# Kernel optimization log

Measured on AMD Instinct MI355X. Metric: run time of the kernel, lower is better.

## Reference

```python
import jax, jax.numpy as jnp
import numpy as np

H = 125      # LSTM hidden per direction
MLP = 100    # hidden_MLP
N = 1024     # sentence length


def _lstm_dir(x, wih, whh, bih, bhh, reverse):
    # x: [n, din]; torch gate order i, f, g, o
    b = bih + bhh
    def step(carry, xt):
        h, c = carry
        g = xt @ wih.T + h @ whh.T + b
        i, f, gg, o = jnp.split(g, 4)
        c = jax.nn.sigmoid(f) * c + jax.nn.sigmoid(i) * jnp.tanh(gg)
        h = jax.nn.sigmoid(o) * jnp.tanh(c)
        return (h, c), h
    z = jnp.zeros((H,), x.dtype)
    _, hs = jax.lax.scan(step, (z, z), x, reverse=reverse)
    return hs  # [n, H]


def _bilstm(x, pf, pb):
    return jnp.concatenate([_lstm_dir(x, *pf, reverse=False),
                            _lstm_dir(x, *pb, reverse=True)], axis=-1)


def setup_inputs() -> dict:
    key = jax.random.key(0)
    ks = iter(jax.random.split(key, 32))
    p = lambda shape, s=0.1: jax.random.normal(next(ks), shape, jnp.float32) * s
    inp = {}
    inp["word_idx"] = jax.random.randint(next(ks), (1, N), 0, 15948)
    inp["pos_idx"] = jax.random.randint(next(ks), (1, N), 0, 47)
    inp["true_tree_heads"] = jax.random.randint(next(ks), (N,), 0, N)
    inp["word_emb"] = p((15948, 100), 1.0)
    inp["pos_emb"] = p((47, 25), 1.0)
    for l, din in ((0, 125), (1, 250)):
        for d in ("f", "b"):
            inp[f"w_ih_{l}{d}"] = p((4 * H, din))
            inp[f"w_hh_{l}{d}"] = p((4 * H, H))
            inp[f"b_ih_{l}{d}"] = p((4 * H,))
            inp[f"b_hh_{l}{d}"] = p((4 * H,))
    inp["w1"] = p((MLP, 2 * H)); inp["b1"] = p((MLP,))
    inp["w2"] = p((MLP, 2 * H)); inp["b2"] = p((MLP,))
    inp["w3"] = p((MLP,)); inp["b3"] = p(())
    return inp


def reference(word_idx, pos_idx, true_tree_heads, word_emb, pos_emb,
              w_ih_0f, w_hh_0f, b_ih_0f, b_hh_0f,
              w_ih_0b, w_hh_0b, b_ih_0b, b_hh_0b,
              w_ih_1f, w_hh_1f, b_ih_1f, b_hh_1f,
              w_ih_1b, w_hh_1b, b_ih_1b, b_hh_1b,
              w1, b1, w2, b2, w3, b3):
    # embeddings: [n, 125]
    emb = jnp.concatenate([word_emb[word_idx[0]], pos_emb[pos_idx[0]]], axis=-1)
    h0 = _bilstm(emb, (w_ih_0f, w_hh_0f, b_ih_0f, b_hh_0f),
                 (w_ih_0b, w_hh_0b, b_ih_0b, b_hh_0b))            # [n, 250]
    h1 = _bilstm(h0, (w_ih_1f, w_hh_1f, b_ih_1f, b_hh_1f),
                 (w_ih_1b, w_hh_1b, b_ih_1b, b_hh_1b))            # [n, 250]
    heads = h1 @ w1.T + b1   # [n, 100]
    mods = h1 @ w2.T + b2    # [n, 100]
    # tag_scores[h, m] = layer3(tanh(heads[h] + mods[m])), diagonal = -inf
    s = jnp.tanh(heads[:, None, :] + mods[None, :, :])            # [n, n, 100]
    scores = jnp.einsum('hmd,d->hm', s, w3) + b3
    n = scores.shape[0]
    return jnp.where(jnp.eye(n, dtype=bool), -jnp.inf, scores)
```

## Files before the change

### kernel.cpp

```cpp
#include <hip/hip_runtime.h>
#include <hip/hip_bf16.h>

#define H 125
#define G4 500
#define NN 1024
#define DMLP 100

#define SCL1 (-1.4426950408889634f)
#define SCL2 (-2.8853900817779268f)

typedef __attribute__((ext_vector_type(4))) float f32x4;
typedef __attribute__((ext_vector_type(4))) int   i32x4;
typedef __attribute__((ext_vector_type(8))) int   i32x8;

__device__ __forceinline__ float frcp(float x) { return __builtin_amdgcn_rcpf(x); }
__device__ __forceinline__ float fexp2(float x) {
    float r;
    asm("v_exp_f32 %0, %1" : "=v"(r) : "v"(x));
    return r;
}

__device__ __forceinline__ float bf16_quant(float v) {
    return __bfloat162float(__float2bfloat16(v));
}

__global__ __launch_bounds__(512) void ingemm4a_k(
    const int* __restrict__ wid, const int* __restrict__ pid,
    const float* __restrict__ wemb, const float* __restrict__ pemb,
    const float* __restrict__ wf, const float* __restrict__ bif, const float* __restrict__ bhf,
    const float* __restrict__ wb, const float* __restrict__ bib, const float* __restrict__ bhb,
    float* __restrict__ xg4f, float* __restrict__ xg4b)
{
    __shared__ float xs[8][125];
    const int dir = blockIdx.y;
    const float* __restrict__ w  = dir ? wb  : wf;
    const float* __restrict__ bi = dir ? bib : bif;
    const float* __restrict__ bh = dir ? bhb : bhf;
    float* __restrict__ xg       = dir ? xg4b : xg4f;

    const int t0  = blockIdx.x * 8;
    const int tid = threadIdx.x;
    for (int i = tid; i < 8 * 125; i += 512) {
        int r = i / 125, k = i - r * 125;
        int t = t0 + r;
        xs[r][k] = (k < 100) ? wemb[wid[t] * 100 + k] : pemb[pid[t] * 25 + (k - 100)];
    }
    __syncthreads();

    if (tid < G4) {
        const int g = tid / 125;
        const int u = tid - g * 125;
        const float sg = (g == 2) ? SCL2 : SCL1;
        const float* wr = w + tid * 125;
        float base = bi[tid] + bh[tid];
        float acc[8];
#pragma unroll
        for (int tt = 0; tt < 8; ++tt) acc[tt] = base;
        for (int k = 0; k < 125; ++k) {
            float wv = wr[k];
#pragma unroll
            for (int tt = 0; tt < 8; ++tt) acc[tt] += wv * xs[tt][k];
        }
#pragma unroll
        for (int tt = 0; tt < 8; ++tt) xg[(t0 + tt) * 512 + u * 4 + g] = acc[tt] * sg;
    } else {
        const int qq = tid - G4;
#pragma unroll
        for (int tt = 0; tt < 8; ++tt) xg[(t0 + tt) * 512 + G4 + qq] = 0.f;
    }
}

__global__ __launch_bounds__(512) void ingemm4_k(
    const float* __restrict__ x,
    const float* __restrict__ wf, const float* __restrict__ bif, const float* __restrict__ bhf,
    const float* __restrict__ wb, const float* __restrict__ bib, const float* __restrict__ bhb,
    float* __restrict__ xg4f, float* __restrict__ xg4b)
{
    __shared__ float xs[8][250];
    const int dir = blockIdx.y;
    const float* __restrict__ w  = dir ? wb  : wf;
    const float* __restrict__ bi = dir ? bib : bif;
    const float* __restrict__ bh = dir ? bhb : bhf;
    float* __restrict__ xg       = dir ? xg4b : xg4f;

    const int t0  = blockIdx.x * 8;
    const int tid = threadIdx.x;
    for (int i = tid; i < 8 * 250; i += 512) {
        int r = i / 250;
        xs[r][i - r * 250] = x[t0 * 250 + i];
    }
    __syncthreads();

    if (tid < G4) {
        const int g = tid / 125;
        const int u = tid - g * 125;
        const float sg = (g == 2) ? SCL2 : SCL1;
        const float* wr = w + tid * 250;
        float base = bi[tid] + bh[tid];
        float acc[8];
#pragma unroll
        for (int tt = 0; tt < 8; ++tt) acc[tt] = base;
        for (int k = 0; k < 250; ++k) {
            float wv = wr[k];
#pragma unroll
            for (int tt = 0; tt < 8; ++tt) acc[tt] += wv * xs[tt][k];
        }
#pragma unroll
        for (int tt = 0; tt < 8; ++tt) xg[(t0 + tt) * 512 + u * 4 + g] = acc[tt] * sg;
    } else {
        const int qq = tid - G4;
#pragma unroll
        for (int tt = 0; tt < 8; ++tt) xg[(t0 + tt) * 512 + G4 + qq] = 0.f;
    }
}

__global__ __launch_bounds__(64) void whhprep8_k(
    const float* __restrict__ whh_f, const float* __restrict__ whh_b,
    int* __restrict__ out)
{
    const int dir = blockIdx.y;
    const float* __restrict__ whh = dir ? whh_b : whh_f;
    const int tg = blockIdx.x;
    const int l  = threadIdx.x;
    const int R  = tg * 16 + (l & 15);
    const int u  = R >> 2, g = R & 3;
    const float sg = (g == 2) ? SCL2 : SCL1;
    const int kb = (l >> 4) * 32;
    float f[32];
#pragma unroll
    for (int e = 0; e < 32; ++e) {
        const int k = kb + e;
        f[e] = (u < H && k < H) ? whh[(g * H + u) * H + k] * sg : 0.f;
    }
    int* dst = out + ((dir * 32 + tg) * 64 + l) * 8;
#pragma unroll
    for (int j = 0; j < 8; ++j) {
        int lo = __builtin_amdgcn_cvt_pk_fp8_f32(f[4 * j + 0], f[4 * j + 1], 0,  false);
        int wv = __builtin_amdgcn_cvt_pk_fp8_f32(f[4 * j + 2], f[4 * j + 3], lo, true);
        dst[j] = wv;
    }
}

__global__ __launch_bounds__(1024, 1) void lstm_scan8_k(
    const float* __restrict__ xg_f, const float* __restrict__ xg_b,
    const int* __restrict__ whhA,
    float* __restrict__ hout)
{
    __shared__ __align__(16) unsigned char hb8[2][128];
    const int dir = blockIdx.x;
    const float* __restrict__ xg = dir ? xg_b : xg_f;
    const int col = dir ? H : 0;

    const int tid = threadIdx.x;
    const int w = tid >> 6;
    const int l = tid & 63;
    const int q = l >> 4;
    const int c = l & 15;

    const i32x8* Ab = (const i32x8*)whhA;
    i32x8 A0 = Ab[(dir * 32 + w * 2 + 0) * 64 + l];
    i32x8 A1 = Ab[(dir * 32 + w * 2 + 1) * 64 + l];

    if (tid < 128) { hb8[0][tid] = 0; hb8[1][tid] = 0; }
    __syncthreads();

    const int rsel = c & 1;
    const int usel = 8 * w + 4 * rsel + q;
    const bool writer = (c < 2);
    const int xoff = 32 * w + 16 * rsel + 4 * q;

    float cst = 0.f;
    int pp = 0;
    auto T = [&](int s) { return dir ? (NN - 1 - s) : s; };

    auto LOADX = [&](int s_) -> f32x4 {
        const int sc = (s_ < NN) ? s_ : NN - 1;
        return *(const f32x4*)(xg + T(sc) * 512 + xoff);
    };

    auto STEP = [&](int t, f32x4 x) {
        const unsigned char* hr = hb8[pp] + 32 * q;
        i32x4 blo = *(const i32x4*)hr;
        i32x4 bhi = *(const i32x4*)(hr + 16);
        i32x8 B;
        B[0] = blo[0]; B[1] = blo[1]; B[2] = blo[2]; B[3] = blo[3];
        B[4] = bhi[0]; B[5] = bhi[1]; B[6] = bhi[2]; B[7] = bhi[3];
        f32x4 a0 = __builtin_amdgcn_mfma_scale_f32_16x16x128_f8f6f4(
            A0, B, x, 0, 0, 0, 0x7F7F7F7F, 0, 0x7F7F7F7F);
        f32x4 a1 = __builtin_amdgcn_mfma_scale_f32_16x16x128_f8f6f4(
            A1, B, x, 0, 0, 0, 0x7F7F7F7F, 0, 0x7F7F7F7F);
        f32x4 gv = rsel ? a1 : a0;

        const float ai = frcp(1.f + fexp2(gv.x));
        const float af = frcp(1.f + fexp2(gv.y));
        const float ag = 2.f * frcp(1.f + fexp2(gv.z)) - 1.f;
        const float ao = frcp(1.f + fexp2(gv.w));
        cst = af * cst + ai * ag;
        const float th = 2.f * frcp(1.f + fexp2(cst * SCL2)) - 1.f;
        const float hv = ao * th;
        if (writer) {
            int pk = __builtin_amdgcn_cvt_pk_fp8_f32(hv, 0.f, 0, false);
            hb8[pp ^ 1][usel] = (unsigned char)(pk & 0xFF);
        }
        asm volatile("s_waitcnt lgkmcnt(0)" ::: "memory");
        __builtin_amdgcn_s_barrier();
        __builtin_amdgcn_sched_barrier(0);
        if (writer && usel < H) hout[t * 250 + col + usel] = hv;
        pp ^= 1;
    };

    f32x4 p0 = LOADX(0), p1 = LOADX(1);
#pragma unroll 1
    for (int s = 0; s < NN; s += 4) {
        f32x4 n0 = LOADX(s + 2), n1 = LOADX(s + 3);
        STEP(T(s),     p0);
        STEP(T(s + 1), p1);
        p0 = LOADX(s + 4); p1 = LOADX(s + 5);
        STEP(T(s + 2), n0);
        STEP(T(s + 3), n1);
    }
}

__global__ __launch_bounds__(256) void headmod_k(
    const float* __restrict__ h1,
    const float* __restrict__ w1, const float* __restrict__ b1,
    const float* __restrict__ w2, const float* __restrict__ b2,
    float* __restrict__ heads, float* __restrict__ mods)
{
    __shared__ float xs[8][250];
    const int t0  = blockIdx.x * 8;
    const int tid = threadIdx.x;
    for (int i = tid; i < 8 * 250; i += 256) {
        int r = i / 250;
        xs[r][i - r * 250] = h1[t0 * 250 + i];
    }
    __syncthreads();

    int d; const float* w; float bb; float* o;
    if (tid < DMLP)                          { d = tid;       w = w1 + d * 250; bb = b1[d]; o = heads; }
    else if (tid >= 128 && tid < 128 + DMLP) { d = tid - 128; w = w2 + d * 250; bb = b2[d]; o = mods;  }
    else return;

    float acc[8];
#pragma unroll
    for (int tt = 0; tt < 8; ++tt) acc[tt] = bb;
    for (int k = 0; k < 250; ++k) {
        float wv = w[k];
#pragma unroll
        for (int tt = 0; tt < 8; ++tt) acc[tt] += wv * xs[tt][k];
    }
#pragma unroll
    for (int tt = 0; tt < 8; ++tt) o[(t0 + tt) * DMLP + d] = acc[tt];
}

__global__ __launch_bounds__(256) void scores_k(
    const float* __restrict__ heads, const float* __restrict__ mods,
    const float* __restrict__ w3, const float* __restrict__ b3,
    float* __restrict__ out)
{
    __shared__ __align__(16) float hh[16][DMLP];
    __shared__ __align__(16) float mm[16][DMLP];
    __shared__ __align__(16) float ws3[DMLP];
    const int bh = blockIdx.y * 16, bm = blockIdx.x * 16;
    const int tid = threadIdx.x;
    for (int i = tid; i < 16 * DMLP; i += 256) {
        int r = i / DMLP, d = i - r * DMLP;
        hh[r][d] = heads[(bh + r) * DMLP + d];
        mm[r][d] = mods[(bm + r) * DMLP + d];
    }
    if (tid < DMLP) ws3[tid] = w3[tid];
    __syncthreads();

    const int tx = tid & 15, ty = tid >> 4;
    const f32x4* h4 = (const f32x4*)hh[ty];
    const f32x4* m4 = (const f32x4*)mm[tx];
    const f32x4* w4 = (const f32x4*)ws3;
    float acc = 0.f;
#pragma unroll
    for (int qq = 0; qq < DMLP / 4; ++qq) {
        f32x4 v  = h4[qq] + m4[qq];
        f32x4 wv = w4[qq];
#pragma unroll
        for (int e = 0; e < 4; ++e) {
            float th = 2.f * frcp(1.f + fexp2(v[e] * SCL2)) - 1.f;
            acc += wv[e] * th;
        }
    }
    acc += b3[0];
    const int hrow = bh + ty, mcol = bm + tx;
    float v = (hrow == mcol) ? -3.3895313892515355e38f : bf16_quant(acc);
    out[hrow * NN + mcol] = v;
}

extern "C" void kernel_launch(void* const* d_in, const int* in_sizes, int n_in,
                              void* d_out, int out_size, void* d_ws, size_t ws_size,
                              hipStream_t stream)
{
    const int*   wid   = (const int*)d_in[0];
    const int*   pid   = (const int*)d_in[1];
    const float* wemb  = (const float*)d_in[3];
    const float* pemb  = (const float*)d_in[4];
    const float* wih0f = (const float*)d_in[5];
    const float* whh0f = (const float*)d_in[6];
    const float* bih0f = (const float*)d_in[7];
    const float* bhh0f = (const float*)d_in[8];
    const float* wih0b = (const float*)d_in[9];
    const float* whh0b = (const float*)d_in[10];
    const float* bih0b = (const float*)d_in[11];
    const float* bhh0b = (const float*)d_in[12];
    const float* wih1f = (const float*)d_in[13];
    const float* whh1f = (const float*)d_in[14];
    const float* bih1f = (const float*)d_in[15];
    const float* bhh1f = (const float*)d_in[16];
    const float* wih1b = (const float*)d_in[17];
    const float* whh1b = (const float*)d_in[18];
    const float* bih1b = (const float*)d_in[19];
    const float* bhh1b = (const float*)d_in[20];
    const float* w1    = (const float*)d_in[21];
    const float* b1    = (const float*)d_in[22];
    const float* w2    = (const float*)d_in[23];
    const float* b2    = (const float*)d_in[24];
    const float* w3    = (const float*)d_in[25];
    const float* b3    = (const float*)d_in[26];

    float* ws    = (float*)d_ws;
    float* xgf   = ws;
    float* xgb   = ws + 524288;
    float* h0    = ws + 1048576;
    float* h1    = ws + 1304576;
    float* hd    = ws + 1560576;
    float* md    = ws + 1662976;
    int*   whhA0 = (int*)(ws + 1765376);
    int*   whhA1 = (int*)(ws + 1798144);

    whhprep8_k<<<dim3(32, 2), 64, 0, stream>>>(whh0f, whh0b, whhA0);
    whhprep8_k<<<dim3(32, 2), 64, 0, stream>>>(whh1f, whh1b, whhA1);

    ingemm4a_k<<<dim3(NN / 8, 2), 512, 0, stream>>>(
        wid, pid, wemb, pemb,
        wih0f, bih0f, bhh0f, wih0b, bih0b, bhh0b, xgf, xgb);

    lstm_scan8_k<<<2, 1024, 0, stream>>>(xgf, xgb, whhA0, h0);

    ingemm4_k<<<dim3(NN / 8, 2), 512, 0, stream>>>(
        h0, wih1f, bih1f, bhh1f, wih1b, bih1b, bhh1b, xgf, xgb);

    lstm_scan8_k<<<2, 1024, 0, stream>>>(xgf, xgb, whhA1, h1);

    headmod_k<<<NN / 8, 256, 0, stream>>>(h1, w1, b1, w2, b2, hd, md);

    scores_k<<<dim3(NN / 16, NN / 16), 256, 0, stream>>>(hd, md, w3, b3, (float*)d_out);
}
```

Before: 1.077 ms.

## Move LSTM gate nonlinearities to first two waves via shared gate buffer

The scan kernel now has writer lanes store raw MFMA gate pre-activations to shared memory, then after a barrier only threads 0-127 (two waves) compute the sigmoid/tanh cell update and write the fp8 hidden state. This drops the double-buffered h and adds a second barrier per step. The aim is to shrink the divergent per-lane activation work on the serial critical path, at the cost of an extra LDS round trip and barrier each timestep.

```diff
diff --git a/kernel.cpp b/kernel.cpp
--- a/kernel.cpp
+++ b/kernel.cpp
@@ -141,12 +141,13 @@
     }
 }
 
-__global__ __launch_bounds__(1024, 1) void lstm_scan8_k(
+__global__ __launch_bounds__(1024, 1) void lstm_scan9_k(
     const float* __restrict__ xg_f, const float* __restrict__ xg_b,
     const int* __restrict__ whhA,
     float* __restrict__ hout)
 {
-    __shared__ __align__(16) unsigned char hb8[2][128];
+    __shared__ __align__(16) unsigned char hb8[128];
+    __shared__ __align__(16) float gates[128 * 4];
     const int dir = blockIdx.x;
     const float* __restrict__ xg = dir ? xg_b : xg_f;
     const int col = dir ? H : 0;
@@ -161,16 +162,14 @@
     i32x8 A0 = Ab[(dir * 32 + w * 2 + 0) * 64 + l];
     i32x8 A1 = Ab[(dir * 32 + w * 2 + 1) * 64 + l];
 
-    if (tid < 128) { hb8[0][tid] = 0; hb8[1][tid] = 0; }
-    __syncthreads();
-
-    const int rsel = c & 1;
-    const int usel = 8 * w + 4 * rsel + q;
+    if (tid < 128) hb8[tid] = 0;
+    __syncthreads();
+
+    const int usel = 8 * w + 4 * (c & 1) + q;
     const bool writer = (c < 2);
-    const int xoff = 32 * w + 16 * rsel + 4 * q;
+    const int xoff = 32 * w + 16 * (c & 1) + 4 * q;
 
     float cst = 0.f;
-    int pp = 0;
     auto T = [&](int s) { return dir ? (NN - 1 - s) : s; };
 
     auto LOADX = [&](int s_) -> f32x4 {
@@ -179,34 +178,34 @@
     };
 
     auto STEP = [&](int t, f32x4 x) {
-        const unsigned char* hr = hb8[pp] + 32 * q;
-        i32x4 blo = *(const i32x4*)hr;
-        i32x4 bhi = *(const i32x4*)(hr + 16);
-        i32x8 B;
-        B[0] = blo[0]; B[1] = blo[1]; B[2] = blo[2]; B[3] = blo[3];
-        B[4] = bhi[0]; B[5] = bhi[1]; B[6] = bhi[2]; B[7] = bhi[3];
+        i32x8 B = *(const i32x8*)(hb8 + 32 * q);
         f32x4 a0 = __builtin_amdgcn_mfma_scale_f32_16x16x128_f8f6f4(
             A0, B, x, 0, 0, 0, 0x7F7F7F7F, 0, 0x7F7F7F7F);
         f32x4 a1 = __builtin_amdgcn_mfma_scale_f32_16x16x128_f8f6f4(
             A1, B, x, 0, 0, 0, 0x7F7F7F7F, 0, 0x7F7F7F7F);
-        f32x4 gv = rsel ? a1 : a0;
-
-        const float ai = frcp(1.f + fexp2(gv.x));
-        const float af = frcp(1.f + fexp2(gv.y));
-        const float ag = 2.f * frcp(1.f + fexp2(gv.z)) - 1.f;
-        const float ao = frcp(1.f + fexp2(gv.w));
-        cst = af * cst + ai * ag;
-        const float th = 2.f * frcp(1.f + fexp2(cst * SCL2)) - 1.f;
-        const float hv = ao * th;
         if (writer) {
-            int pk = __builtin_amdgcn_cvt_pk_fp8_f32(hv, 0.f, 0, false);
-            hb8[pp ^ 1][usel] = (unsigned char)(pk & 0xFF);
+            f32x4 gv = (c & 1) ? a1 : a0;
+            *(f32x4*)(gates + 4 * usel) = gv;
         }
         asm volatile("s_waitcnt lgkmcnt(0)" ::: "memory");
         __builtin_amdgcn_s_barrier();
         __builtin_amdgcn_sched_barrier(0);
-        if (writer && usel < H) hout[t * 250 + col + usel] = hv;
-        pp ^= 1;
+        if (tid < 128) {
+            f32x4 g = *(const f32x4*)(gates + 4 * tid);
+            const float ai = frcp(1.f + fexp2(g.x));
+            const float af = frcp(1.f + fexp2(g.y));
+            const float ag = 2.f * frcp(1.f + fexp2(g.z)) - 1.f;
+            const float ao = frcp(1.f + fexp2(g.w));
+            cst = af * cst + ai * ag;
+            const float th = 2.f * frcp(1.f + fexp2(cst * SCL2)) - 1.f;
+            const float hv = ao * th;
+            int pk = __builtin_amdgcn_cvt_pk_fp8_f32(hv, 0.f, 0, false);
+            hb8[tid] = (unsigned char)(pk & 0xFF);
+            if (tid < H) hout[t * 250 + col + tid] = hv;
+        }
+        asm volatile("s_waitcnt lgkmcnt(0)" ::: "memory");
+        __builtin_amdgcn_s_barrier();
+        __builtin_amdgcn_sched_barrier(0);
     };
 
     f32x4 p0 = LOADX(0), p1 = LOADX(1);
@@ -340,12 +339,12 @@
         wid, pid, wemb, pemb,
         wih0f, bih0f, bhh0f, wih0b, bih0b, bhh0b, xgf, xgb);
 
-    lstm_scan8_k<<<2, 1024, 0, stream>>>(xgf, xgb, whhA0, h0);
+    lstm_scan9_k<<<2, 1024, 0, stream>>>(xgf, xgb, whhA0, h0);
 
     ingemm4_k<<<dim3(NN / 8, 2), 512, 0, stream>>>(
         h0, wih1f, bih1f, bhh1f, wih1b, bih1b, bhh1b, xgf, xgb);
 
-    lstm_scan8_k<<<2, 1024, 0, stream>>>(xgf, xgb, whhA1, h1);
+    lstm_scan9_k<<<2, 1024, 0, stream>>>(xgf, xgb, whhA1, h1);
 
     headmod_k<<<NN / 8, 256, 0, stream>>>(h1, w1, b1, w2, b2, hd, md);
 
```

Measured after the change: 1.032 ms. 4.1% less time.
